# Kernel tuning notes

Hardware: AMD Instinct MI355X
Metric: run time of the kernel (lower is better)

Reference implementation:

```python
import jax, jax.numpy as jnp
import numpy as np

B, S, D = 2, 2048, 2048
VOCAB = 32000
CUTOFFS = [1000, 2000, 5000, VOCAB]  # torch appends vocab_size
N_CLUSTERS = 3
HEAD_SIZE = CUTOFFS[0] + N_CLUSTERS  # 1003
LN_EPS = 1e-5
INIT = 0.02


def setup_inputs() -> dict:
    key = jax.random.key(0)
    ks = jax.random.split(key, 10)
    inp = {
        "x": jax.random.normal(ks[0], (B, S, D), dtype=jnp.float32),
        "targets": jax.random.randint(ks[1], (B, S), 0, VOCAB, dtype=jnp.int32),
        "gamma": jnp.ones((D,), jnp.float32),
        "beta": jnp.zeros((D,), jnp.float32),
        "head_w": jax.random.normal(ks[2], (HEAD_SIZE, D), jnp.float32) * INIT,
    }
    # tail clusters: hsz = D // 4**i, osz = cutoffs[i] - cutoffs[i-1]
    for i in range(1, 4):
        hsz = D // (4 ** i)
        osz = CUTOFFS[i] - CUTOFFS[i - 1]
        inp[f"t{i}_w1"] = jax.random.normal(ks[2 + 2 * i], (hsz, D), jnp.float32) * INIT
        inp[f"t{i}_w2"] = jax.random.normal(ks[3 + 2 * i], (osz, hsz), jnp.float32) * INIT
    return inp


def reference(x, targets, gamma, beta, head_w, t1_w1, t1_w2, t2_w1, t2_w2, t3_w1, t3_w2):
    # LayerNorm over last dim
    mu = jnp.mean(x, axis=-1, keepdims=True)
    var = jnp.mean(jnp.square(x - mu), axis=-1, keepdims=True)
    xn = (x - mu) * jax.lax.rsqrt(var + LN_EPS) * gamma + beta

    # shift: predict token t+1 from hidden t
    h = xn[:, :-1, :].reshape(-1, x.shape[-1])      # [N, D]
    lbl = targets[:, 1:].reshape(-1)                # [N]
    n = h.shape[0]
    rows = jnp.arange(n)

    # head: shortlist (first cutoff) + one logit per tail cluster
    head_lp = jax.nn.log_softmax(h @ head_w.T, axis=-1)  # [N, 1003]
    out = head_lp[rows, jnp.clip(lbl, 0, CUTOFFS[0] - 1)]

    tails = [(t1_w1, t1_w2), (t2_w1, t2_w2), (t3_w1, t3_w2)]
    for i, (w1, w2) in enumerate(tails):
        low, high = CUTOFFS[i], CUTOFFS[i + 1]
        tail_lp = jax.nn.log_softmax((h @ w1.T) @ w2.T, axis=-1)  # [N, osz]
        rel = jnp.clip(lbl - low, 0, high - low - 1)
        lp = head_lp[:, CUTOFFS[0] + i] + tail_lp[rows, rel]
        out = jnp.where((lbl >= low) & (lbl < high), lp, out)

    return -jnp.mean(out)  # NLL loss, matches .loss of AdaptiveLogSoftmaxWithLoss
```

## Files before the change

### kernel.cpp

```cpp
#include <hip/hip_runtime.h>
#include <hip/hip_bf16.h>
#include <math.h>

#define BB 2
#define SS 2048
#define DD 2048
#define NR (BB*(SS-1))
#define NRP 4096
#define MT_LD 768
#define MT_P2 512
#define MT_P3 640

#define L2E 1.4426950408889634f
#define LN2F 0.6931471805599453f
#define LSE_SHIFT 4.0f
#define LSE_NC (-LSE_SHIFT * L2E)
#define WSCALE 16.0f
#define WINV   0.0625f

typedef short  bh8   __attribute__((ext_vector_type(8)));
typedef float  f32x4 __attribute__((ext_vector_type(4)));
typedef long   l64x2 __attribute__((ext_vector_type(2)));

__device__ inline float bfl(unsigned short b) { return __uint_as_float(((unsigned)b) << 16); }
__device__ inline float expsh(float v) { return __builtin_amdgcn_exp2f(fmaf(v, L2E, LSE_NC)); }

__device__ inline float block_sum256(float v) {
    __shared__ float tmp[4];
    #pragma unroll
    for (int o = 32; o > 0; o >>= 1) v += __shfl_down(v, o, 64);
    int lane = threadIdx.x & 63, w = threadIdx.x >> 6;
    if (lane == 0) tmp[w] = v;
    __syncthreads();
    float r = tmp[0] + tmp[1] + tmp[2] + tmp[3];
    __syncthreads();
    return r;
}

__device__ inline unsigned pack_fp8x4(float a, float b, float c, float d) {
    unsigned r = 0;
    r = __builtin_amdgcn_cvt_pk_fp8_f32(a, b, r, false);
    r = __builtin_amdgcn_cvt_pk_fp8_f32(c, d, r, true);
    return r;
}

struct CastSegs {
    const float* src[7];
    void* dst[7];
    int n_src[7];
    int n_tot[7];
    int b0[7];
    int isfp8[7];
    float scl[7];
};
struct AParams {
    const float* x; const float* gamma; const float* beta;
    unsigned char* h8;
    CastSegs sg; int castBlocks;
    const int* targets;
    int *relH, *rel1, *rel2, *rel3;
    float *S0, *S1, *S2, *out;
};

__global__ __launch_bounds__(256) void stageA(AParams p) {
    int blk = blockIdx.x, tid = threadIdx.x;
    if (blk < NRP) {
        int n = blk;
        unsigned char* hr = p.h8 + (size_t)n * DD;
        if (n >= NR) { *(uint2*)(hr + tid * 8) = make_uint2(0,0); return; }
        int b = n / (SS - 1), t = n % (SS - 1);
        const float4* xr = (const float4*)(p.x + (size_t)(b * SS + t) * DD);
        float4 a = xr[tid * 2];
        float4 c = xr[tid * 2 + 1];
        float sum = a.x + a.y + a.z + a.w + c.x + c.y + c.z + c.w;
        sum = block_sum256(sum);
        float mu = sum * (1.0f / DD);
        float d[8] = {a.x-mu, a.y-mu, a.z-mu, a.w-mu, c.x-mu, c.y-mu, c.z-mu, c.w-mu};
        float sq = 0.f;
        #pragma unroll
        for (int i = 0; i < 8; ++i) sq += d[i] * d[i];
        sq = block_sum256(sq);
        float rstd = rsqrtf(sq * (1.0f / DD) + 1e-5f);
        const float4* g4 = (const float4*)p.gamma;
        const float4* be4 = (const float4*)p.beta;
        float4 g1 = g4[tid*2], g2 = g4[tid*2+1];
        float4 b1 = be4[tid*2], b2 = be4[tid*2+1];
        float gg[8] = {g1.x,g1.y,g1.z,g1.w,g2.x,g2.y,g2.z,g2.w};
        float bb[8] = {b1.x,b1.y,b1.z,b1.w,b2.x,b2.y,b2.z,b2.w};
        float o[8];
        #pragma unroll
        for (int i = 0; i < 8; ++i) o[i] = d[i] * rstd * gg[i] + bb[i];
        uint2 pk;
        pk.x = pack_fp8x4(o[0], o[1], o[2], o[3]);
        pk.y = pack_fp8x4(o[4], o[5], o[6], o[7]);
        *(uint2*)(hr + tid * 8) = pk;
        return;
    }
    blk -= NRP;
    if (blk < p.castBlocks) {
        int k = 0;
        #pragma unroll
        for (int i = 1; i < 7; ++i) if (blk >= p.sg.b0[i]) k = i;
        int i4 = (blk - p.sg.b0[k]) * 1024 + tid * 4;
        if (i4 >= p.sg.n_tot[k]) return;
        float4 v = make_float4(0.f,0.f,0.f,0.f);
        if (i4 < p.sg.n_src[k]) v = *(const float4*)(p.sg.src[k] + i4);
        if (p.sg.isfp8[k]) {
            unsigned pk = pack_fp8x4(v.x * WSCALE, v.y * WSCALE, v.z * WSCALE, v.w * WSCALE);
            *(unsigned*)((unsigned char*)p.sg.dst[k] + i4) = pk;
        } else {
            float sc = p.sg.scl[k];
            __align__(8) __hip_bfloat16 o[4] = {
                __float2bfloat16(v.x * sc), __float2bfloat16(v.y * sc),
                __float2bfloat16(v.z * sc), __float2bfloat16(v.w * sc)};
            *(uint2*)((__hip_bfloat16*)p.sg.dst[k] + i4) = *(uint2*)o;
        }
        return;
    }
    blk -= p.castBlocks;
    int n = blk * 256 + tid;
    if (n >= NRP) return;
    int lbl = -1;
    if (n < NR) {
        int b = n / (SS - 1), t = n % (SS - 1);
        lbl = p.targets[b * SS + t + 1];
    }
    bool v = n < NR;
    p.relH[n] = v ? (lbl < 1000 ? lbl : 999) : -1;
    int r1 = lbl - 1000;  p.rel1[n] = v ? (r1 < 0 ? 0 : (r1 > 999   ? 999   : r1)) : -1;
    int r2 = lbl - 2000;  p.rel2[n] = v ? (r2 < 0 ? 0 : (r2 > 2999  ? 2999  : r2)) : -1;
    int r3 = lbl - 5000;  p.rel3[n] = v ? (r3 < 0 ? 0 : (r3 > 26999 ? 26999 : r3)) : -1;
    p.S0[n] = 0.f; p.S1[n] = 0.f; p.S2[n] = 0.f;
    if (n == 0) p.out[0] = 0.f;
}

__global__ __launch_bounds__(256) void megaF(
        const unsigned char* __restrict__ A,
        const unsigned char* __restrict__ W,
        __hip_bfloat16* __restrict__ megaT,
        const int* __restrict__ relH,
        float* __restrict__ S0, float* __restrict__ aux) {
    __shared__ __align__(16) unsigned char smF[2][16384];
    int tid = threadIdx.x, wv = tid >> 6, lane = tid & 63;
    int row0 = blockIdx.y * 128, col0 = blockIdx.x * 128;
    int wrow = (wv >> 1) * 64, wcol = (wv & 1) * 64;
    f32x4 acc[4][4];
    #pragma unroll
    for (int i = 0; i < 4; ++i)
        #pragma unroll
        for (int j = 0; j < 4; ++j) acc[i][j] = (f32x4){0.f,0.f,0.f,0.f};
    int sr = lane >> 2;
    int kp = (((lane & 3) ^ (sr & 3)) * 16);
    int mrow = lane & 15;
    int qx = (((lane >> 4) ^ (lane & 3)) * 16);

    auto stage = [&](int buf, int k0) {
        #pragma unroll
        for (int i = 0; i < 2; ++i) {
            int chunk = wv * 2 + i;
            int r = chunk * 16 + sr;
            const void* ga = A + (size_t)(row0 + r) * DD + k0 + kp;
            const void* gw = W + (size_t)(col0 + r) * DD + k0 + kp;
            void* la = (char*)&smF[buf][0]    + chunk * 1024 + lane * 16;
            void* lw = (char*)&smF[buf][8192] + chunk * 1024 + lane * 16;
            __builtin_amdgcn_global_load_lds(
                (const __attribute__((address_space(1))) void*)ga,
                (__attribute__((address_space(3))) void*)la, 16, 0, 0);
            __builtin_amdgcn_global_load_lds(
                (const __attribute__((address_space(1))) void*)gw,
                (__attribute__((address_space(3))) void*)lw, 16, 0, 0);
        }
    };

    stage(0, 0);
    asm volatile("s_waitcnt vmcnt(0)" ::: "memory");
    __builtin_amdgcn_s_barrier();
    __builtin_amdgcn_sched_barrier(0);
    int cur = 0;
    for (int k0 = 0; k0 < DD; k0 += 64) {
        if (k0 + 64 < DD) stage(cur ^ 1, k0 + 64);
        const unsigned char* As = &smF[cur][0];
        const unsigned char* Ws = &smF[cur][8192];
        l64x2 af[4], bfr[4];
        #pragma unroll
        for (int t = 0; t < 4; ++t) {
            af[t]  = *(const l64x2*)(As + (wrow + t*16 + mrow) * 64 + qx);
            bfr[t] = *(const l64x2*)(Ws + (wcol + t*16 + mrow) * 64 + qx);
        }
        #pragma unroll
        for (int s = 0; s < 2; ++s)
            #pragma unroll
            for (int i = 0; i < 4; ++i)
                #pragma unroll
                for (int j = 0; j < 4; ++j)
                    acc[i][j] = __builtin_amdgcn_mfma_f32_16x16x32_fp8_fp8(
                        af[i][s], bfr[j][s], acc[i][j], 0, 0, 0);
        asm volatile("s_waitcnt vmcnt(0) lgkmcnt(0)" ::: "memory");
        __builtin_amdgcn_s_barrier();
        __builtin_amdgcn_sched_barrier(0);
        cur ^= 1;
    }
    int ccol = lane & 15, g = lane >> 4;
    if (blockIdx.x < 8) {
        int grs[4][4], rh[4][4];
        float ps[4][4];
        #pragma unroll
        for (int i = 0; i < 4; ++i)
            #pragma unroll
            for (int r = 0; r < 4; ++r) {
                grs[i][r] = row0 + wrow + i*16 + g*4 + r;
                rh[i][r] = relH[grs[i][r]];
                ps[i][r] = 0.f;
            }
        #pragma unroll
        for (int i = 0; i < 4; ++i)
            #pragma unroll
            for (int j = 0; j < 4; ++j) {
                int gc = col0 + wcol + j*16 + ccol;
                bool inr = gc < 1003;
                #pragma unroll
                for (int r = 0; r < 4; ++r) {
                    float v = acc[i][j][r] * WINV;
                    if (gc == rh[i][r]) aux[grs[i][r]*8 + 0] = v;
                    if (gc >= 1000 && gc < 1003) aux[grs[i][r]*8 + 2 + (gc - 1000)] = v;
                    ps[i][r] += inr ? expsh(v) : 0.f;
                }
            }
        #pragma unroll
        for (int off = 1; off < 16; off <<= 1)
            #pragma unroll
            for (int i = 0; i < 4; ++i)
                #pragma unroll
                for (int r = 0; r < 4; ++r) ps[i][r] += __shfl_xor(ps[i][r], off, 64);
        if (ccol == 0)
            #pragma unroll
            for (int i = 0; i < 4; ++i)
                #pragma unroll
                for (int r = 0; r < 4; ++r) atomicAdd(&S0[grs[i][r]], ps[i][r]);
    } else {
        int cb = col0 - 1024 + wcol;
        #pragma unroll
        for (int i = 0; i < 4; ++i) {
            size_t gr0 = row0 + wrow + i*16 + g*4;
            #pragma unroll
            for (int j = 0; j < 4; ++j) {
                size_t gc = cb + j*16 + ccol;
                #pragma unroll
                for (int r = 0; r < 4; ++r)
                    megaT[(gr0 + r) * MT_LD + gc] = __float2bfloat16(acc[i][j][r] * WINV);
            }
        }
    }
}

__device__ void tail_gemm(const __hip_bfloat16* A, int lda,
        const __hip_bfloat16* W, int K, int bx, int by, int validCols,
        const int* rel, float* S, float* tgt, char* sm) {
    __hip_bfloat16* As = (__hip_bfloat16*)sm;
    __hip_bfloat16* Ws = (__hip_bfloat16*)(sm + 4096);
    int tid = threadIdx.x, wv = tid >> 6, lane = tid & 63;
    int row0 = by * 64, col0 = bx * 128;
    int wrow = (wv >> 1) * 32, wcol = (wv & 1) * 64;
    f32x4 acc[2][4];
    #pragma unroll
    for (int i = 0; i < 2; ++i)
        #pragma unroll
        for (int j = 0; j < 4; ++j) acc[i][j] = (f32x4){0.f,0.f,0.f,0.f};
    int sr = lane >> 2;
    int sk = (((lane & 3) ^ (sr & 3)) * 8);
    int mrow = lane & 15;
    int qx = (((lane >> 4) ^ (lane & 3)) * 16);

    for (int k0 = 0; k0 < K; k0 += 32) {
        __syncthreads();
        #pragma unroll
        for (int i = 0; i < 3; ++i) {
            int c = wv * 3 + i;
            const __hip_bfloat16* gsrc;
            char* ldst;
            if (c < 4) {
                gsrc = A + (size_t)(row0 + c * 16 + sr) * lda + k0 + sk;
                ldst = (char*)As + c * 1024 + lane * 16;
            } else {
                int cw = c - 4;
                gsrc = W + (size_t)(col0 + cw * 16 + sr) * K + k0 + sk;
                ldst = (char*)Ws + cw * 1024 + lane * 16;
            }
            __builtin_amdgcn_global_load_lds(
                (const __attribute__((address_space(1))) void*)gsrc,
                (__attribute__((address_space(3))) void*)ldst, 16, 0, 0);
        }
        __syncthreads();
        bh8 af[2], bfr[4];
        #pragma unroll
        for (int t = 0; t < 2; ++t)
            af[t] = *(const bh8*)((const char*)As + (wrow + t*16 + mrow) * 64 + qx);
        #pragma unroll
        for (int t = 0; t < 4; ++t)
            bfr[t] = *(const bh8*)((const char*)Ws + (wcol + t*16 + mrow) * 64 + qx);
        #pragma unroll
        for (int i = 0; i < 2; ++i)
            #pragma unroll
            for (int j = 0; j < 4; ++j)
                acc[i][j] = __builtin_amdgcn_mfma_f32_16x16x32_bf16(af[i], bfr[j], acc[i][j], 0, 0, 0);
    }
    int ccol = lane & 15, g = lane >> 4;
    int grs[2][4], rh[2][4];
    float p[2][4];
    #pragma unroll
    for (int i = 0; i < 2; ++i)
        #pragma unroll
        for (int r = 0; r < 4; ++r) {
            grs[i][r] = row0 + wrow + i*16 + g*4 + r;
            rh[i][r] = rel[grs[i][r]];
            p[i][r] = 0.f;
        }
    #pragma unroll
    for (int i = 0; i < 2; ++i)
        #pragma unroll
        for (int j = 0; j < 4; ++j) {
            int gc = col0 + wcol + j*16 + ccol;
            bool inr = gc < validCols;
            #pragma unroll
            for (int r = 0; r < 4; ++r) {
                float v = acc[i][j][r];
                if (gc == rh[i][r]) tgt[grs[i][r]] = v;
                p[i][r] += inr ? expsh(v) : 0.f;
            }
        }
    #pragma unroll
    for (int off = 1; off < 16; off <<= 1)
        #pragma unroll
        for (int i = 0; i < 2; ++i)
            #pragma unroll
            for (int r = 0; r < 4; ++r) p[i][r] += __shfl_xor(p[i][r], off, 64);
    if (ccol == 0)
        #pragma unroll
        for (int i = 0; i < 2; ++i)
            #pragma unroll
            for (int r = 0; r < 4; ++r) atomicAdd(&S[grs[i][r]], p[i][r]);
}

#define T3_TILES 1688
#define T3_SPLIT 32
#define T3_TPC   53
__device__ void t3_partial_body(const __hip_bfloat16* megaT,
        const __hip_bfloat16* w2b, float* pS, int idx, int tid, float* red ) {
    int rg = idx >> 5, cs = idx & 31;
    int wv = tid >> 6, lane = tid & 63;
    int q = lane >> 4, cm = lane & 15;
    int row0 = rg * 64;
    bh8 af[4];
    #pragma unroll
    for (int h = 0; h < 4; ++h)
        af[h] = *(const bh8*)(megaT + (size_t)(row0 + h*16 + cm) * MT_LD + MT_P3 + q * 8);
    int tile0 = cs * T3_TPC;
    int tile1 = tile0 + T3_TPC; if (tile1 > T3_TILES) tile1 = T3_TILES;
    float s[4][4];
    #pragma unroll
    for (int h = 0; h < 4; ++h)
        #pragma unroll
        for (int r = 0; r < 4; ++r) s[h][r] = 0.f;
    int ot = tile0 + wv;
    auto baddr = [&](int t) {
        int tc = t < tile1 ? t : tile1 - 1;
        return (const bh8*)(w2b + (size_t)(tc * 16 + cm) * 32 + q * 8);
    };
    bh8 p0 = *baddr(ot), p1 = *baddr(ot + 4), p2 = *baddr(ot + 8), p3 = *baddr(ot + 12);
    for (; ot < tile1; ot += 4) {
        bh8 bcur = p0;
        p0 = p1; p1 = p2; p2 = p3;
        int otn = ot + 16;
        if (otn < tile1)
            p3 = *(const bh8*)(w2b + (size_t)(otn * 16 + cm) * 32 + q * 8);
        f32x4 c[4];
        #pragma unroll
        for (int h = 0; h < 4; ++h)
            c[h] = __builtin_amdgcn_mfma_f32_16x16x32_bf16(af[h], bcur, (f32x4){0,0,0,0}, 0, 0, 0);
        #pragma unroll
        for (int h = 0; h < 4; ++h)
            #pragma unroll
            for (int r = 0; r < 4; ++r) s[h][r] += __builtin_amdgcn_exp2f(c[h][r]);
    }
    #pragma unroll
    for (int off = 1; off < 16; off <<= 1)
        #pragma unroll
        for (int h = 0; h < 4; ++h)
            #pragma unroll
            for (int r = 0; r < 4; ++r) s[h][r] += __shfl_xor(s[h][r], off, 64);
    if (cm == 0)
        #pragma unroll
        for (int h = 0; h < 4; ++h)
            #pragma unroll
            for (int r = 0; r < 4; ++r)
                red[wv * 64 + h*16 + q*4 + r] = s[h][r];
    __syncthreads();
    if (tid < 64)
        pS[(size_t)(row0 + tid) * T3_SPLIT + cs] =
            red[tid] + red[64 + tid] + red[128 + tid] + red[192 + tid];
}

__device__ void t3_gather_body(const __hip_bfloat16* megaT, const __hip_bfloat16* w2b,
        const int* rel3, float* tt2, int idx, int tid) {
    int n = idx * 256 + tid;
    if (n >= NR) return;
    int rc = rel3[n];
    const unsigned short* pa = (const unsigned short*)(megaT + (size_t)n * MT_LD + MT_P3);
    const unsigned short* pw = (const unsigned short*)(w2b + (size_t)rc * 32);
    float acc = 0.f;
    #pragma unroll
    for (int k = 0; k < 32; ++k) acc += bfl(pa[k]) * bfl(pw[k]);
    tt2[n] = acc;
}

#define NT3 (64 * T3_SPLIT)
__global__ __launch_bounds__(256) void fatT3(const __hip_bfloat16* __restrict__ megaT,
        const __hip_bfloat16* __restrict__ w2b3, const int* __restrict__ rel3,
        float* __restrict__ pS3, float* __restrict__ tt2) {
    __shared__ __align__(16) float red[256];
    int idx = blockIdx.x, tid = threadIdx.x;
    if (idx < NT3) { t3_partial_body(megaT, w2b3, pS3, idx, tid, red); return; }
    t3_gather_body(megaT, w2b3, rel3, tt2, idx - NT3, tid);
}

#define NT1 512
#define NT2 1536
__global__ __launch_bounds__(256) void fatT12(const __hip_bfloat16* __restrict__ megaT,
        const __hip_bfloat16* __restrict__ t1w2b, const __hip_bfloat16* __restrict__ t2w2b,
        const int* __restrict__ rel1, const int* __restrict__ rel2,
        float* __restrict__ S1, float* __restrict__ S2,
        float* __restrict__ tt0, float* __restrict__ tt1) {
    __shared__ __align__(16) char sm[12288];
    int idx = blockIdx.x, tid = threadIdx.x;
    if (idx < NT1) { tail_gemm(megaT, MT_LD, t1w2b, 512, idx % 8, idx / 8, 1000, rel1, S1, tt0, sm); return; }
    idx -= NT1;
    tail_gemm(megaT + MT_P2, MT_LD, t2w2b, 128, idx % 24, idx / 24, 3000, rel2, S2, tt1, sm);
    (void)tid;
}

__global__ __launch_bounds__(256) void final_kernel(const float* __restrict__ aux,
        const int* __restrict__ targets,
        const float* __restrict__ S0, const float* __restrict__ S1, const float* __restrict__ S2,
        const float* __restrict__ pS3,
        const float* __restrict__ tt0, const float* __restrict__ tt1, const float* __restrict__ tt2,
        float* __restrict__ out) {
    int n = blockIdx.x * 256 + threadIdx.x;
    float local = 0.f;
    if (n < NR) {
        int b = n / (SS - 1), t = n % (SS - 1);
        int lbl = targets[b * SS + t + 1];
        float lse = logf(S0[n]) + LSE_SHIFT;
        float o;
        if (lbl < 1000)      o = aux[n*8 + 0] - lse;
        else if (lbl < 2000) o = (aux[n*8 + 2] - lse) + (tt0[n] - (logf(S1[n]) + LSE_SHIFT));
        else if (lbl < 5000) o = (aux[n*8 + 3] - lse) + (tt1[n] - (logf(S2[n]) + LSE_SHIFT));
        else {
            float S3 = 0.f;
            const float4* p4 = (const float4*)(pS3 + (size_t)n * T3_SPLIT);
            #pragma unroll
            for (int c = 0; c < T3_SPLIT/4; ++c) {
                float4 v = p4[c];
                S3 += v.x + v.y + v.z + v.w;
            }
            S3 -= 8.0f;
            o = (aux[n*8 + 4] - lse) + (tt2[n] * LN2F - logf(S3));
        }
        local = o;
    }
    local = block_sum256(local);
    if (threadIdx.x == 0) atomicAdd(out, -local / (float)NR);
}

extern "C" void kernel_launch(void* const* d_in, const int* in_sizes, int n_in,
                              void* d_out, int out_size, void* d_ws, size_t ws_size,
                              hipStream_t stream) {
    const float* x      = (const float*)d_in[0];
    const int*   targets= (const int*)d_in[1];
    const float* gamma  = (const float*)d_in[2];
    const float* beta   = (const float*)d_in[3];
    const float* head_w = (const float*)d_in[4];
    const float* t1_w1  = (const float*)d_in[5];
    const float* t1_w2  = (const float*)d_in[6];
    const float* t2_w1  = (const float*)d_in[7];
    const float* t2_w2  = (const float*)d_in[8];
    const float* t3_w1  = (const float*)d_in[9];
    const float* t3_w2  = (const float*)d_in[10];
    (void)in_sizes; (void)n_in; (void)out_size; (void)ws_size;

    char* base = (char*)d_ws;
    size_t off = 0;
    auto ab = [&](size_t nbytes) { char* p = base + off; off += (nbytes + 15) & ~(size_t)15; return p; };
    unsigned char* h8     = (unsigned char*)ab((size_t)NRP * DD);
    unsigned char* w1cat8 = (unsigned char*)ab((size_t)1792 * DD);
    __hip_bfloat16* megaT = (__hip_bfloat16*)ab((size_t)NRP * MT_LD * 2);
    __hip_bfloat16* t1w2b = (__hip_bfloat16*)ab((size_t)1024 * 512 * 2);
    __hip_bfloat16* t2w2b = (__hip_bfloat16*)ab((size_t)3072 * 128 * 2);
    __hip_bfloat16* w2b3  = (__hip_bfloat16*)ab((size_t)27008 * 32 * 2);
    float* aux = (float*)ab((size_t)NRP * 8 * 4);
    float* pS3 = (float*)ab((size_t)NRP * T3_SPLIT * 4);
    float* S0  = (float*)ab(NRP * 4);
    float* S1  = (float*)ab(NRP * 4);
    float* S2  = (float*)ab(NRP * 4);
    int* relH  = (int*)ab(NRP * 4);
    int* rel1  = (int*)ab(NRP * 4);
    int* rel2  = (int*)ab(NRP * 4);
    int* rel3  = (int*)ab(NRP * 4);
    float* tt0 = (float*)ab(NRP * 4);
    float* tt1 = (float*)ab(NRP * 4);
    float* tt2 = (float*)ab(NRP * 4);

    AParams p;
    p.x = x; p.gamma = gamma; p.beta = beta; p.h8 = h8;
    p.targets = targets;
    p.relH = relH; p.rel1 = rel1; p.rel2 = rel2; p.rel3 = rel3;
    p.S0 = S0; p.S1 = S1; p.S2 = S2; p.out = (float*)d_out;
    const float* srcs[7] = {head_w, t1_w1, t2_w1, t3_w1, t1_w2, t2_w2, t3_w2};
    void* dsts[7] = {w1cat8, w1cat8 + (size_t)1024*2048, w1cat8 + (size_t)1536*2048,
                     w1cat8 + (size_t)1664*2048, t1w2b, t2w2b, w2b3};
    int nsrc[7] = {1003*2048, 512*2048, 128*2048, 32*2048, 1000*512, 3000*128, 27000*32};
    int ntot[7] = {1024*2048, 512*2048, 128*2048, 128*2048, 1024*512, 3072*128, 27008*32};
    int isf8[7] = {1, 1, 1, 1, 0, 0, 0};
    float scls[7] = {1.f, 1.f, 1.f, 1.f, 1.0f, 1.0f, L2E};
    int blk = 0;
    for (int i = 0; i < 7; ++i) {
        p.sg.src[i] = srcs[i]; p.sg.dst[i] = dsts[i];
        p.sg.n_src[i] = nsrc[i]; p.sg.n_tot[i] = ntot[i];
        p.sg.isfp8[i] = isf8[i];
        p.sg.scl[i] = scls[i];
        p.sg.b0[i] = blk;
        blk += (ntot[i] + 1023) / 1024;
    }
    p.castBlocks = blk;

    stageA<<<NRP + blk + 16, 256, 0, stream>>>(p);
    megaF<<<dim3(14, 32), 256, 0, stream>>>(h8, w1cat8, megaT, relH, S0, aux);
    fatT3<<<NT3 + 16, 256, 0, stream>>>(megaT, w2b3, rel3, pS3, tt2);
    fatT12<<<NT1 + NT2, 256, 0, stream>>>(megaT, t1w2b, t2w2b, rel1, rel2, S1, S2, tt0, tt1);
    final_kernel<<<16, 256, 0, stream>>>(aux, targets, S0, S1, S2, pS3, tt0, tt1, tt2, (float*)d_out);
}
```

Baseline: 194.9 us.

## Halve megaF row tile to 64 and merge tail-cluster kernels into one launch

The fp8 GEMM kernel now uses 64x128 tiles instead of 128x128, doubling the grid from 448 to 896 blocks so more of the GPU's compute units have work, at the cost of lower per-block operand reuse. The separate fatT3 and fatT12 kernels are merged into a single fatC launch that dispatches by block index to the t3 partial, t1, t2 and t3 gather bodies. This removes one launch and its inter-kernel gap, and lets the different tail workloads run at the same time.

```diff
diff --git a/kernel.cpp b/kernel.cpp
--- a/kernel.cpp
+++ b/kernel.cpp
@@ -140,13 +140,13 @@
         __hip_bfloat16* __restrict__ megaT,
         const int* __restrict__ relH,
         float* __restrict__ S0, float* __restrict__ aux) {
-    __shared__ __align__(16) unsigned char smF[2][16384];
+    __shared__ __align__(16) unsigned char smF[2][12288];
     int tid = threadIdx.x, wv = tid >> 6, lane = tid & 63;
-    int row0 = blockIdx.y * 128, col0 = blockIdx.x * 128;
-    int wrow = (wv >> 1) * 64, wcol = (wv & 1) * 64;
-    f32x4 acc[4][4];
-    #pragma unroll
-    for (int i = 0; i < 4; ++i)
+    int row0 = blockIdx.y * 64, col0 = blockIdx.x * 128;
+    int wrow = (wv >> 1) * 32, wcol = (wv & 1) * 64;
+    f32x4 acc[2][4];
+    #pragma unroll
+    for (int i = 0; i < 2; ++i)
         #pragma unroll
         for (int j = 0; j < 4; ++j) acc[i][j] = (f32x4){0.f,0.f,0.f,0.f};
     int sr = lane >> 2;
@@ -155,17 +155,20 @@
     int qx = (((lane >> 4) ^ (lane & 3)) * 16);
 
     auto stage = [&](int buf, int k0) {
+        {
+            int r = wv * 16 + sr;
+            const void* ga = A + (size_t)(row0 + r) * DD + k0 + kp;
+            void* la = (char*)&smF[buf][0] + wv * 1024 + lane * 16;
+            __builtin_amdgcn_global_load_lds(
+                (const __attribute__((address_space(1))) void*)ga,
+                (__attribute__((address_space(3))) void*)la, 16, 0, 0);
+        }
         #pragma unroll
         for (int i = 0; i < 2; ++i) {
             int chunk = wv * 2 + i;
             int r = chunk * 16 + sr;
-            const void* ga = A + (size_t)(row0 + r) * DD + k0 + kp;
             const void* gw = W + (size_t)(col0 + r) * DD + k0 + kp;
-            void* la = (char*)&smF[buf][0]    + chunk * 1024 + lane * 16;
-            void* lw = (char*)&smF[buf][8192] + chunk * 1024 + lane * 16;
-            __builtin_amdgcn_global_load_lds(
-                (const __attribute__((address_space(1))) void*)ga,
-                (__attribute__((address_space(3))) void*)la, 16, 0, 0);
+            void* lw = (char*)&smF[buf][4096] + chunk * 1024 + lane * 16;
             __builtin_amdgcn_global_load_lds(
                 (const __attribute__((address_space(1))) void*)gw,
                 (__attribute__((address_space(3))) void*)lw, 16, 0, 0);
@@ -180,17 +183,18 @@
     for (int k0 = 0; k0 < DD; k0 += 64) {
         if (k0 + 64 < DD) stage(cur ^ 1, k0 + 64);
         const unsigned char* As = &smF[cur][0];
-        const unsigned char* Ws = &smF[cur][8192];
-        l64x2 af[4], bfr[4];
-        #pragma unroll
-        for (int t = 0; t < 4; ++t) {
+        const unsigned char* Ws = &smF[cur][4096];
+        l64x2 af[2], bfr[4];
+        #pragma unroll
+        for (int t = 0; t < 2; ++t)
             af[t]  = *(const l64x2*)(As + (wrow + t*16 + mrow) * 64 + qx);
+        #pragma unroll
+        for (int t = 0; t < 4; ++t)
             bfr[t] = *(const l64x2*)(Ws + (wcol + t*16 + mrow) * 64 + qx);
-        }
         #pragma unroll
         for (int s = 0; s < 2; ++s)
             #pragma unroll
-            for (int i = 0; i < 4; ++i)
+            for (int i = 0; i < 2; ++i)
                 #pragma unroll
                 for (int j = 0; j < 4; ++j)
                     acc[i][j] = __builtin_amdgcn_mfma_f32_16x16x32_fp8_fp8(
@@ -202,10 +206,10 @@
     }
     int ccol = lane & 15, g = lane >> 4;
     if (blockIdx.x < 8) {
-        int grs[4][4], rh[4][4];
-        float ps[4][4];
-        #pragma unroll
-        for (int i = 0; i < 4; ++i)
+        int grs[2][4], rh[2][4];
+        float ps[2][4];
+        #pragma unroll
+        for (int i = 0; i < 2; ++i)
             #pragma unroll
             for (int r = 0; r < 4; ++r) {
                 grs[i][r] = row0 + wrow + i*16 + g*4 + r;
@@ -213,7 +217,7 @@
                 ps[i][r] = 0.f;
             }
         #pragma unroll
-        for (int i = 0; i < 4; ++i)
+        for (int i = 0; i < 2; ++i)
             #pragma unroll
             for (int j = 0; j < 4; ++j) {
                 int gc = col0 + wcol + j*16 + ccol;
@@ -229,18 +233,18 @@
         #pragma unroll
         for (int off = 1; off < 16; off <<= 1)
             #pragma unroll
-            for (int i = 0; i < 4; ++i)
+            for (int i = 0; i < 2; ++i)
                 #pragma unroll
                 for (int r = 0; r < 4; ++r) ps[i][r] += __shfl_xor(ps[i][r], off, 64);
         if (ccol == 0)
             #pragma unroll
-            for (int i = 0; i < 4; ++i)
+            for (int i = 0; i < 2; ++i)
                 #pragma unroll
                 for (int r = 0; r < 4; ++r) atomicAdd(&S0[grs[i][r]], ps[i][r]);
     } else {
         int cb = col0 - 1024 + wcol;
         #pragma unroll
-        for (int i = 0; i < 4; ++i) {
+        for (int i = 0; i < 2; ++i) {
             size_t gr0 = row0 + wrow + i*16 + g*4;
             #pragma unroll
             for (int j = 0; j < 4; ++j) {
@@ -414,28 +418,23 @@
 }
 
 #define NT3 (64 * T3_SPLIT)
-__global__ __launch_bounds__(256) void fatT3(const __hip_bfloat16* __restrict__ megaT,
-        const __hip_bfloat16* __restrict__ w2b3, const int* __restrict__ rel3,
-        float* __restrict__ pS3, float* __restrict__ tt2) {
-    __shared__ __align__(16) float red[256];
-    int idx = blockIdx.x, tid = threadIdx.x;
-    if (idx < NT3) { t3_partial_body(megaT, w2b3, pS3, idx, tid, red); return; }
-    t3_gather_body(megaT, w2b3, rel3, tt2, idx - NT3, tid);
-}
-
 #define NT1 512
 #define NT2 1536
-__global__ __launch_bounds__(256) void fatT12(const __hip_bfloat16* __restrict__ megaT,
+__global__ __launch_bounds__(256) void fatC(const __hip_bfloat16* __restrict__ megaT,
         const __hip_bfloat16* __restrict__ t1w2b, const __hip_bfloat16* __restrict__ t2w2b,
-        const int* __restrict__ rel1, const int* __restrict__ rel2,
-        float* __restrict__ S1, float* __restrict__ S2,
-        float* __restrict__ tt0, float* __restrict__ tt1) {
+        const __hip_bfloat16* __restrict__ w2b3,
+        const int* __restrict__ rel1, const int* __restrict__ rel2, const int* __restrict__ rel3,
+        float* __restrict__ S1, float* __restrict__ S2, float* __restrict__ pS3,
+        float* __restrict__ tt0, float* __restrict__ tt1, float* __restrict__ tt2) {
     __shared__ __align__(16) char sm[12288];
     int idx = blockIdx.x, tid = threadIdx.x;
+    if (idx < NT3) { t3_partial_body(megaT, w2b3, pS3, idx, tid, (float*)sm); return; }
+    idx -= NT3;
     if (idx < NT1) { tail_gemm(megaT, MT_LD, t1w2b, 512, idx % 8, idx / 8, 1000, rel1, S1, tt0, sm); return; }
     idx -= NT1;
-    tail_gemm(megaT + MT_P2, MT_LD, t2w2b, 128, idx % 24, idx / 24, 3000, rel2, S2, tt1, sm);
-    (void)tid;
+    if (idx < NT2) { tail_gemm(megaT + MT_P2, MT_LD, t2w2b, 128, idx % 24, idx / 24, 3000, rel2, S2, tt1, sm); return; }
+    idx -= NT2;
+    t3_gather_body(megaT, w2b3, rel3, tt2, idx, tid);
 }
 
 __global__ __launch_bounds__(256) void final_kernel(const float* __restrict__ aux,
@@ -533,8 +532,8 @@
     p.castBlocks = blk;
 
     stageA<<<NRP + blk + 16, 256, 0, stream>>>(p);
-    megaF<<<dim3(14, 32), 256, 0, stream>>>(h8, w1cat8, megaT, relH, S0, aux);
-    fatT3<<<NT3 + 16, 256, 0, stream>>>(megaT, w2b3, rel3, pS3, tt2);
-    fatT12<<<NT1 + NT2, 256, 0, stream>>>(megaT, t1w2b, t2w2b, rel1, rel2, S1, S2, tt0, tt1);
+    megaF<<<dim3(14, 64), 256, 0, stream>>>(h8, w1cat8, megaT, relH, S0, aux);
+    fatC<<<NT3 + NT1 + NT2 + 16, 256, 0, stream>>>(megaT, t1w2b, t2w2b, w2b3,
+            rel1, rel2, rel3, S1, S2, pS3, tt0, tt1, tt2);
     final_kernel<<<16, 256, 0, stream>>>(aux, targets, S0, S1, S2, pS3, tt0, tt1, tt2, (float*)d_out);
 }
```

Result: faster. 187.2 us (-3.9%).
